# Kernel optimization log

Measured on AMD Instinct MI355X. Metric: run time of the kernel, lower is better.

## Reference

```python
import jax, jax.numpy as jnp
import numpy as np

B, S, H, NH = 4, 2048, 768, 12
HD = H // NH

def _ln(x, g, b, eps=1e-5):
    m = jnp.mean(x, -1, keepdims=True)
    v = jnp.mean((x - m) ** 2, -1, keepdims=True)
    return (x - m) * jax.lax.rsqrt(v + eps) * g + b

def setup_inputs() -> dict:
    key = jax.random.key(0)
    ks = jax.random.split(key, 16)
    s = 0.02
    return {
        "x": jax.random.normal(ks[0], (B, S, H), jnp.float32),
        "prev_state": jax.random.normal(ks[1], (B, S, H), jnp.float32),
        "mask": jax.random.randint(ks[2], (B,), 0, 2).astype(bool),
        # depthwise conv1d (groups=H, k=3): torch weight [H, 1, 3] == OIH
        "conv_dw_w": jax.random.normal(ks[3], (H, 1, 3), jnp.float32) * s,
        "conv_dw_b": jnp.zeros((H,), jnp.float32),
        # pointwise conv1d (k=1) stored as [out, in]
        "conv_pw_w": jax.random.normal(ks[4], (H, H), jnp.float32) * s,
        "conv_pw_b": jnp.zeros((H,), jnp.float32),
        "cn_g": jnp.ones((H,), jnp.float32), "cn_b": jnp.zeros((H,), jnp.float32),
        "Wq": jax.random.normal(ks[5], (H, H), jnp.float32) * s, "bq": jnp.zeros((H,), jnp.float32),
        "Wk": jax.random.normal(ks[6], (H, H), jnp.float32) * s, "bk": jnp.zeros((H,), jnp.float32),
        "Wv": jax.random.normal(ks[7], (H, H), jnp.float32) * s, "bv": jnp.zeros((H,), jnp.float32),
        "Wo": jax.random.normal(ks[8], (H, H), jnp.float32) * s, "bo": jnp.zeros((H,), jnp.float32),
        "pn_g": jnp.ones((H,), jnp.float32), "pn_b": jnp.zeros((H,), jnp.float32),
        "Wpost": jax.random.normal(ks[9], (H, H), jnp.float32) * s, "bpost": jnp.zeros((H,), jnp.float32),
        "Wg": jax.random.normal(ks[10], (1, 2 * H), jnp.float32) * s, "bg": jnp.zeros((1,), jnp.float32),
    }

def reference(x, prev_state, mask, conv_dw_w, conv_dw_b, conv_pw_w, conv_pw_b,
              cn_g, cn_b, Wq, bq, Wk, bk, Wv, bv, Wo, bo,
              pn_g, pn_b, Wpost, bpost, Wg, bg):
    # ---- bridge: depthwise conv (k=3) -> pointwise conv (k=1) -> GELU -> LN ----
    mem_t = prev_state.transpose(0, 2, 1)  # [B, H, S]
    dw = jax.lax.conv_general_dilated(
        mem_t, conv_dw_w, window_strides=(1,), padding=[(1, 1)],
        feature_group_count=H, dimension_numbers=("NCH", "OIH", "NCH")) + conv_dw_b[None, :, None]
    pw = jnp.einsum("bhs,oh->bos", dw, conv_pw_w) + conv_pw_b[None, :, None]
    bridged = jax.nn.gelu(pw, approximate=False).transpose(0, 2, 1)  # [B, S, H]
    bridged = _ln(bridged, cn_g, cn_b)
    # ---- cross attention: q from x, k/v from bridged memory (nope, non-causal) ----
    q = (jnp.einsum("bsh,oh->bso", x, Wq) + bq).reshape(B, S, NH, HD)
    k = (jnp.einsum("bsh,oh->bso", bridged, Wk) + bk).reshape(B, S, NH, HD)
    v = (jnp.einsum("bsh,oh->bso", bridged, Wv) + bv).reshape(B, S, NH, HD)
    scores = jnp.einsum("bqnd,bknd->bnqk", q, k) / np.float32(np.sqrt(HD))
    attn = jax.nn.softmax(scores, axis=-1)
    ao = jnp.einsum("bnqk,bknd->bqnd", attn, v).reshape(B, S, H)
    ao = jnp.einsum("bsh,oh->bso", ao, Wo) + bo
    # ---- post-attn norm, linear, gate, scatter-add back under mask ----
    inj = _ln(ao, pn_g, pn_b)
    inj = jnp.einsum("bsh,oh->bso", inj, Wpost) + bpost
    gate = jax.nn.sigmoid(jnp.einsum("bsh,oh->bso", jnp.concatenate([x, bridged], -1), Wg) + bg)
    gated = gate * jnp.tanh(inj)
    mf = mask.astype(x.dtype)[:, None, None]  # batch-row select == masked scatter-add
    out = x + mf * gated
    # masked MSE aux loss (only over selected rows, as in the original)
    denom = jnp.maximum(mask.sum(), 1).astype(x.dtype) * np.float32(S * H)
    aux = jnp.sum(mf * (bridged - x) ** 2) / denom
    return out, aux
```

## Files before the change

### kernel.cpp

```cpp
#include <hip/hip_runtime.h>
#include <math.h>

#define B_ 4
#define S_ 2048
#define H_ 768
#define NH_ 12
#define HD_ 64
#define BSH (B_ * S_ * H_)
#define NROWS (B_ * S_)
#define WSZ (H_ * H_)

typedef __attribute__((ext_vector_type(8))) short bf16x8;
typedef __attribute__((ext_vector_type(4))) short s16x4;
typedef __attribute__((ext_vector_type(4))) float f32x4;
typedef __attribute__((ext_vector_type(2))) unsigned u32x2;

__device__ __forceinline__ short f2bf(float f) {
  union { float f; unsigned u; } x; x.f = f;
  unsigned r = x.u + 0x7FFF + ((x.u >> 16) & 1);
  return (short)(r >> 16);
}
__device__ __forceinline__ float bf2f(short s) {
  union { unsigned u; float f; } x;
  x.u = ((unsigned)(unsigned short)s) << 16;
  return x.f;
}
__device__ __forceinline__ unsigned bfpack(float lo, float hi) {
  union { float f; unsigned u; } a, b; a.f = lo; b.f = hi;
  return __builtin_amdgcn_perm(b.u, a.u, 0x07060302);
}

typedef __attribute__((address_space(1))) const unsigned int g_u32;
typedef __attribute__((address_space(3))) unsigned int l_u32;
__device__ __forceinline__ void gload16(const void* g, void* l) {
  __builtin_amdgcn_global_load_lds((g_u32*)g, (l_u32*)l, 16, 0, 0);
}

__global__ __launch_bounds__(256) void cvt_x_k(const float* __restrict__ src,
                                               short* __restrict__ dst) {
  int i = (blockIdx.x * 256 + threadIdx.x) * 4;
  float4 v = *(const float4*)(src + i);
  s16x4 o = {f2bf(v.x), f2bf(v.y), f2bf(v.z), f2bf(v.w)};
  *(s16x4*)(dst + i) = o;
}

__global__ __launch_bounds__(256) void cvt6_k(const float* w0, const float* w1,
                                              const float* w2, const float* w3,
                                              const float* w4, const float* w5,
                                              short* __restrict__ dst) {
  int i = (blockIdx.x * 256 + threadIdx.x) * 4;
  int m = i / WSZ;
  int off = i - m * WSZ;
  const float* s = m == 0 ? w0 : m == 1 ? w1 : m == 2 ? w2 : m == 3 ? w3 : m == 4 ? w4 : w5;
  float4 v = *(const float4*)(s + off);
  s16x4 o = {f2bf(v.x), f2bf(v.y), f2bf(v.z), f2bf(v.w)};
  *(s16x4*)(dst + i) = o;
}

__global__ __launch_bounds__(192) void dwconv_k(const float* __restrict__ prev,
                                                const float* __restrict__ w3,
                                                const float* __restrict__ bias,
                                                short* __restrict__ out) {
  int row = blockIdx.x;
  int s = row & (S_ - 1);
  int h = threadIdx.x * 4;
  size_t base = (size_t)row * H_ + h;
  float4 c = *(const float4*)(prev + base);
  float4 wa = *(const float4*)(w3 + h * 3);
  float4 wb = *(const float4*)(w3 + h * 3 + 4);
  float4 wc = *(const float4*)(w3 + h * 3 + 8);
  float4 bi = *(const float4*)(bias + h);
  float4 acc;
  acc.x = bi.x + c.x * wa.y;
  acc.y = bi.y + c.y * wb.x;
  acc.z = bi.z + c.z * wb.w;
  acc.w = bi.w + c.w * wc.z;
  if (s > 0) {
    float4 l = *(const float4*)(prev + base - H_);
    acc.x += l.x * wa.x; acc.y += l.y * wa.w; acc.z += l.z * wb.z; acc.w += l.w * wc.y;
  }
  if (s < S_ - 1) {
    float4 r = *(const float4*)(prev + base + H_);
    acc.x += r.x * wa.z; acc.y += r.y * wb.y; acc.z += r.z * wc.x; acc.w += r.w * wc.w;
  }
  s16x4 o = {f2bf(acc.x), f2bf(acc.y), f2bf(acc.z), f2bf(acc.w)};
  *(s16x4*)(out + base) = o;
}

struct GemmJob {
  const short* A; const short* W; const float* bias; short* C; int act; int tout;
};

__global__ __launch_bounds__(256) void gemm_bf2(GemmJob j0, GemmJob j1, GemmJob j2) {
  GemmJob j = blockIdx.z == 0 ? j0 : (blockIdx.z == 1 ? j1 : j2);
  __shared__ short As[128 * 64];
  __shared__ short Ws[128 * 64];
  int tid = threadIdx.x, lane = tid & 63, w = tid >> 6;
  int wr = w >> 1, wc = w & 1, lm = lane & 15, lq = lane >> 4;
  int m0 = blockIdx.y * 128, n0 = blockIdx.x * 128;
  int srow = lane >> 3;
  int skc = (lane & 7) * 8;
  const short* gA = j.A + (size_t)(m0 + w * 32 + srow) * H_ + skc;
  const short* gW = j.W + (size_t)(n0 + w * 32 + srow) * H_ + skc;
  short* lA = As + w * 2048;
  short* lW = Ws + w * 2048;

  f32x4 acc[4][4];
#pragma unroll
  for (int i = 0; i < 4; ++i)
#pragma unroll
    for (int jj = 0; jj < 4; ++jj) acc[i][jj] = (f32x4){0.f, 0.f, 0.f, 0.f};

  for (int kt = 0; kt < H_; kt += 64) {
    __syncthreads();
#pragma unroll
    for (int c = 0; c < 4; ++c) {
      gload16(gA + kt + (size_t)(c * 8) * H_, lA + c * 512);
      gload16(gW + kt + (size_t)(c * 8) * H_, lW + c * 512);
    }
    __syncthreads();
#pragma unroll
    for (int kk = 0; kk < 2; ++kk) {
      bf16x8 af[4], wf[4];
#pragma unroll
      for (int i = 0; i < 4; ++i)
        af[i] = *(const bf16x8*)&As[(wr * 64 + i * 16 + lm) * 64 + kk * 32 + lq * 8];
#pragma unroll
      for (int jj = 0; jj < 4; ++jj)
        wf[jj] = *(const bf16x8*)&Ws[(wc * 64 + jj * 16 + lm) * 64 + kk * 32 + lq * 8];
#pragma unroll
      for (int i = 0; i < 4; ++i)
#pragma unroll
        for (int jj = 0; jj < 4; ++jj)
          acc[i][jj] = __builtin_amdgcn_mfma_f32_16x16x32_bf16(af[i], wf[jj], acc[i][jj], 0, 0, 0);
    }
  }

  if (!j.tout) {
#pragma unroll
    for (int jj = 0; jj < 4; ++jj) {
      int col = n0 + wc * 64 + jj * 16 + lm;
      float bn = j.bias[col];
#pragma unroll
      for (int i = 0; i < 4; ++i) {
        int mrow = m0 + wr * 64 + i * 16 + lq * 4;
#pragma unroll
        for (int r = 0; r < 4; ++r) {
          float cv = acc[i][jj][r] + bn;
          if (j.act) cv = 0.5f * cv * (1.0f + erff(cv * 0.70710678118f));
          j.C[(size_t)(mrow + r) * H_ + col] = f2bf(cv);
        }
      }
    }
  } else {
    int b = m0 >> 11;
    int sb = (m0 & (S_ - 1)) + wr * 64;
#pragma unroll
    for (int jj = 0; jj < 4; ++jj) {
      int col = n0 + wc * 64 + jj * 16 + lm;
      float bn = j.bias[col];
      short* cp = j.C + ((size_t)(b * H_ + col)) * S_;
#pragma unroll
      for (int i = 0; i < 4; ++i) {
        int s = sb + i * 16 + lq * 4;
        s16x4 pk = {f2bf(acc[i][jj][0] + bn), f2bf(acc[i][jj][1] + bn),
                    f2bf(acc[i][jj][2] + bn), f2bf(acc[i][jj][3] + bn)};
        *(s16x4*)(cp + s) = pk;
      }
    }
  }
}

__global__ __launch_bounds__(256) void ln_bf(const short* __restrict__ X,
                                             short* __restrict__ Y,
                                             const float* __restrict__ g,
                                             const float* __restrict__ bb) {
  int row = blockIdx.x;
  size_t base = (size_t)row * H_;
  int h0 = threadIdx.x, h1 = h0 + 256, h2 = h0 + 512;
  float x0 = bf2f(X[base + h0]), x1 = bf2f(X[base + h1]), x2 = bf2f(X[base + h2]);
  float s = x0 + x1 + x2;
  float s2 = x0 * x0 + x1 * x1 + x2 * x2;
  for (int off = 32; off > 0; off >>= 1) {
    s += __shfl_down(s, off);
    s2 += __shfl_down(s2, off);
  }
  __shared__ float sa[4], sq[4], st[2];
  int wid = threadIdx.x >> 6, lane = threadIdx.x & 63;
  if (lane == 0) { sa[wid] = s; sq[wid] = s2; }
  __syncthreads();
  if (threadIdx.x == 0) {
    float ts = sa[0] + sa[1] + sa[2] + sa[3];
    float ts2 = sq[0] + sq[1] + sq[2] + sq[3];
    float mean = ts * (1.0f / H_);
    float var = ts2 * (1.0f / H_) - mean * mean;
    st[0] = mean;
    st[1] = rsqrtf(var + 1e-5f);
  }
  __syncthreads();
  float mean = st[0], rstd = st[1];
  Y[base + h0] = f2bf((x0 - mean) * rstd * g[h0] + bb[h0]);
  Y[base + h1] = f2bf((x1 - mean) * rstd * g[h1] + bb[h1]);
  Y[base + h2] = f2bf((x2 - mean) * rstd * g[h2] + bb[h2]);
}

__global__ __launch_bounds__(512) void attn3_k(const short* __restrict__ qb,
                                               const short* __restrict__ kb,
                                               const short* __restrict__ vtb,
                                               short* __restrict__ aob) {
  __shared__ short Ks[64 * 72];
  __shared__ short Vt[64 * 72];
  __shared__ short Ps[8 * 16 * 72];
  int tid = threadIdx.x, lane = tid & 63, w = tid >> 6;
  int lm = lane & 15, lq = lane >> 4;
  int b = blockIdx.z, n = blockIdx.y, q0 = blockIdx.x * 128;
  int hoff = n * HD_;

  const short* qrow = qb + ((size_t)(b * S_ + q0 + w * 16 + lm)) * H_ + hoff;
  bf16x8 qf0 = *(const bf16x8*)(qrow + lq * 8);
  bf16x8 qf1 = *(const bf16x8*)(qrow + 32 + lq * 8);

  float l_ = 0.f;
  f32x4 o[4];
#pragma unroll
  for (int i = 0; i < 4; ++i) o[i] = (f32x4){0.f, 0.f, 0.f, 0.f};

  int r0 = tid >> 3, c0 = (tid & 7) * 8;
  const short* kg = kb + ((size_t)(b * S_)) * H_ + hoff;
  const short* vg = vtb + ((size_t)(b * H_ + hoff)) * S_;
  const float C1 = 0.1803368802f;

  bf16x8 kv = *(const bf16x8*)(kg + (size_t)r0 * H_ + c0);
  bf16x8 vv = *(const bf16x8*)(vg + (size_t)r0 * S_ + c0);

  for (int kt = 0; kt < S_; kt += 64) {
    __syncthreads();
    *(bf16x8*)&Ks[r0 * 72 + c0] = kv;
    *(bf16x8*)&Vt[r0 * 72 + c0] = vv;
    __syncthreads();
    if (kt + 64 < S_) {
      kv = *(const bf16x8*)(kg + (size_t)(kt + 64 + r0) * H_ + c0);
      vv = *(const bf16x8*)(vg + (size_t)r0 * S_ + kt + 64 + c0);
    }

    f32x4 st[4];
#pragma unroll
    for (int ni = 0; ni < 4; ++ni) {
      bf16x8 ka0 = *(const bf16x8*)&Ks[(ni * 16 + lm) * 72 + lq * 8];
      bf16x8 ka1 = *(const bf16x8*)&Ks[(ni * 16 + lm) * 72 + 32 + lq * 8];
      f32x4 z = (f32x4){0.f, 0.f, 0.f, 0.f};
      z = __builtin_amdgcn_mfma_f32_16x16x32_bf16(ka0, qf0, z, 0, 0, 0);
      st[ni] = __builtin_amdgcn_mfma_f32_16x16x32_bf16(ka1, qf1, z, 0, 0, 0);
    }

    float rs = 0.f;
#pragma unroll
    for (int ni = 0; ni < 4; ++ni) {
      float p0 = exp2f(st[ni][0] * C1);
      float p1 = exp2f(st[ni][1] * C1);
      float p2 = exp2f(st[ni][2] * C1);
      float p3 = exp2f(st[ni][3] * C1);
      rs += (p0 + p1) + (p2 + p3);
      u32x2 pk = {bfpack(p0, p1), bfpack(p2, p3)};
      *(u32x2*)&Ps[(w * 16 + lm) * 72 + ni * 16 + lq * 4] = pk;
    }
    rs += __shfl_xor(rs, 16);
    rs += __shfl_xor(rs, 32);
    l_ += rs;

    bf16x8 pf0 = *(const bf16x8*)&Ps[(w * 16 + lm) * 72 + lq * 8];
    bf16x8 pf1 = *(const bf16x8*)&Ps[(w * 16 + lm) * 72 + 32 + lq * 8];
#pragma unroll
    for (int nd = 0; nd < 4; ++nd) {
      bf16x8 va0 = *(const bf16x8*)&Vt[(nd * 16 + lm) * 72 + lq * 8];
      bf16x8 va1 = *(const bf16x8*)&Vt[(nd * 16 + lm) * 72 + 32 + lq * 8];
      o[nd] = __builtin_amdgcn_mfma_f32_16x16x32_bf16(va0, pf0, o[nd], 0, 0, 0);
      o[nd] = __builtin_amdgcn_mfma_f32_16x16x32_bf16(va1, pf1, o[nd], 0, 0, 0);
    }
  }

  float inv = 1.0f / l_;
  short* orow = aob + ((size_t)(b * S_ + q0 + w * 16 + lm)) * H_ + hoff;
#pragma unroll
  for (int nd = 0; nd < 4; ++nd) {
    s16x4 pk = {f2bf(o[nd][0] * inv), f2bf(o[nd][1] * inv),
                f2bf(o[nd][2] * inv), f2bf(o[nd][3] * inv)};
    *(s16x4*)(orow + nd * 16 + lq * 4) = pk;
  }
}

__global__ __launch_bounds__(192) void gate_out_k(const float* __restrict__ x,
                                                  const short* __restrict__ br,
                                                  const short* __restrict__ inj,
                                                  const int* __restrict__ mask,
                                                  const float* __restrict__ Wg,
                                                  const float* __restrict__ bg,
                                                  float* __restrict__ out,
                                                  float* __restrict__ paux) {
  int row = blockIdx.x;
  int b = row >> 11;
  size_t base = (size_t)row * H_;
  int h = threadIdx.x * 4;
  float4 xv = *(const float4*)(x + base + h);
  s16x4 brv = *(const s16x4*)(br + base + h);
  s16x4 inv = *(const s16x4*)(inj + base + h);
  float4 wg0 = *(const float4*)(Wg + h);
  float4 wg1 = *(const float4*)(Wg + H_ + h);
  float b0 = bf2f(brv.x), b1 = bf2f(brv.y), b2 = bf2f(brv.z), b3 = bf2f(brv.w);
  float dot = xv.x * wg0.x + xv.y * wg0.y + xv.z * wg0.z + xv.w * wg0.w
            + b0 * wg1.x + b1 * wg1.y + b2 * wg1.z + b3 * wg1.w;
  float d0 = b0 - xv.x, d1 = b1 - xv.y, d2 = b2 - xv.z, d3 = b3 - xv.w;
  float aux = d0 * d0 + d1 * d1 + d2 * d2 + d3 * d3;
  for (int off = 32; off > 0; off >>= 1) {
    dot += __shfl_down(dot, off);
    aux += __shfl_down(aux, off);
  }
  __shared__ float sd[3], sx[3], gsh[2];
  int wid = threadIdx.x >> 6, lane = threadIdx.x & 63;
  if (lane == 0) { sd[wid] = dot; sx[wid] = aux; }
  __syncthreads();
  if (threadIdx.x == 0) {
    float td = sd[0] + sd[1] + sd[2];
    float ta = sx[0] + sx[1] + sx[2];
    gsh[0] = 1.0f / (1.0f + expf(-(td + bg[0])));
    gsh[1] = ta;
  }
  __syncthreads();
  float mf = (mask[b] != 0) ? 1.0f : 0.0f;
  float gm = gsh[0] * mf;
  float v0 = bf2f(inv.x), v1 = bf2f(inv.y), v2 = bf2f(inv.z), v3 = bf2f(inv.w);
  float e0 = __expf(2.f * v0), e1 = __expf(2.f * v1), e2 = __expf(2.f * v2), e3 = __expf(2.f * v3);
  float4 ov;
  ov.x = xv.x + gm * ((e0 - 1.f) / (e0 + 1.f));
  ov.y = xv.y + gm * ((e1 - 1.f) / (e1 + 1.f));
  ov.z = xv.z + gm * ((e2 - 1.f) / (e2 + 1.f));
  ov.w = xv.w + gm * ((e3 - 1.f) / (e3 + 1.f));
  *(float4*)(out + base + h) = ov;
  if (threadIdx.x == 0) paux[row] = mf * gsh[1];
}

__global__ __launch_bounds__(256) void aux_reduce_k(const float* __restrict__ paux,
                                                    const int* __restrict__ mask,
                                                    float* __restrict__ outp) {
  float s = 0.f;
  for (int i = threadIdx.x; i < NROWS; i += 256) s += paux[i];
  for (int off = 32; off > 0; off >>= 1) s += __shfl_down(s, off);
  __shared__ float sw[4];
  int wid = threadIdx.x >> 6, lane = threadIdx.x & 63;
  if (lane == 0) sw[wid] = s;
  __syncthreads();
  if (threadIdx.x == 0) {
    float t = sw[0] + sw[1] + sw[2] + sw[3];
    int nm = (mask[0] != 0) + (mask[1] != 0) + (mask[2] != 0) + (mask[3] != 0);
    if (nm < 1) nm = 1;
    outp[0] = t / ((float)nm * (float)(S_ * H_));
  }
}

extern "C" void kernel_launch(void* const* d_in, const int* in_sizes, int n_in,
                              void* d_out, int out_size, void* d_ws, size_t ws_size,
                              hipStream_t stream) {
  const float* x     = (const float*)d_in[0];
  const float* prev  = (const float*)d_in[1];
  const int*   mask  = (const int*)d_in[2];
  const float* dw_w  = (const float*)d_in[3];
  const float* dw_b  = (const float*)d_in[4];
  const float* pw_w  = (const float*)d_in[5];
  const float* pw_b  = (const float*)d_in[6];
  const float* cn_g  = (const float*)d_in[7];
  const float* cn_b  = (const float*)d_in[8];
  const float* Wq    = (const float*)d_in[9];
  const float* bq    = (const float*)d_in[10];
  const float* Wk    = (const float*)d_in[11];
  const float* bk    = (const float*)d_in[12];
  const float* Wv    = (const float*)d_in[13];
  const float* bv    = (const float*)d_in[14];
  const float* Wo    = (const float*)d_in[15];
  const float* bo    = (const float*)d_in[16];
  const float* pn_g  = (const float*)d_in[17];
  const float* pn_b  = (const float*)d_in[18];
  const float* Wpost = (const float*)d_in[19];
  const float* bpost = (const float*)d_in[20];
  const float* Wg    = (const float*)d_in[21];
  const float* bg    = (const float*)d_in[22];
  float* out = (float*)d_out;

  short* B0 = (short*)d_ws;
  short* B1 = B0 + BSH;
  short* B2 = B1 + BSH;
  short* B3 = B2 + BSH;
  short* B4 = B3 + BSH;
  short* B5 = B4 + BSH;
  short* WW = B5 + BSH;
  float* paux = (float*)(WW + 6 * WSZ);

  dim3 g1(H_ / 128, NROWS / 128, 1);
  dim3 g3(H_ / 128, NROWS / 128, 3);

  GemmJob jpw   = {B1, WW,           pw_b,  B2, 1, 0};
  GemmJob jq    = {B0, WW + WSZ,     bq,    B1, 0, 0};
  GemmJob jk    = {B3, WW + 2 * WSZ, bk,    B4, 0, 0};
  GemmJob jv    = {B3, WW + 3 * WSZ, bv,    B5, 0, 1};
  GemmJob jo    = {B2, WW + 4 * WSZ, bo,    B4, 0, 0};
  GemmJob jpost = {B4, WW + 5 * WSZ, bpost, B5, 0, 0};

  cvt6_k<<<6 * WSZ / 1024, 256, 0, stream>>>(pw_w, Wq, Wk, Wv, Wo, Wpost, WW);
  cvt_x_k<<<BSH / 1024, 256, 0, stream>>>(x, B0);
  dwconv_k<<<NROWS, 192, 0, stream>>>(prev, dw_w, dw_b, B1);
  gemm_bf2<<<g1, 256, 0, stream>>>(jpw, jpw, jpw);
  ln_bf<<<NROWS, 256, 0, stream>>>(B2, B3, cn_g, cn_b);
  gemm_bf2<<<g3, 256, 0, stream>>>(jq, jk, jv);
  attn3_k<<<dim3(S_ / 128, NH_, B_), 512, 0, stream>>>(B1, B4, B5, B2);
  gemm_bf2<<<g1, 256, 0, stream>>>(jo, jo, jo);
  ln_bf<<<NROWS, 256, 0, stream>>>(B4, B4, pn_g, pn_b);
  gemm_bf2<<<g1, 256, 0, stream>>>(jpost, jpost, jpost);
  gate_out_k<<<NROWS, 192, 0, stream>>>(x, B3, B5, mask, Wg, bg, out, paux);
  aux_reduce_k<<<1, 256, 0, stream>>>(paux, mask, out + BSH);
}
```

Before: 419.2 us.

## Add 128x64 GEMM tile for single GEMMs and double query rows per attention wave

```diff
diff --git a/kernel.cpp b/kernel.cpp
--- a/kernel.cpp
+++ b/kernel.cpp
@@ -171,6 +171,69 @@
   }
 }
 
+__global__ __launch_bounds__(256) void gemm_n64(const short* __restrict__ A,
+                                                const short* __restrict__ W,
+                                                const float* __restrict__ bias,
+                                                short* __restrict__ C, int act) {
+  __shared__ short As[128 * 64];
+  __shared__ short Ws[64 * 64];
+  int tid = threadIdx.x, lane = tid & 63, w = tid >> 6;
+  int wm = w >> 1, wn = w & 1, lm = lane & 15, lq = lane >> 4;
+  int m0 = blockIdx.y * 128, n0 = blockIdx.x * 64;
+  const short* gA = A + (size_t)(m0 + w * 32 + (lane >> 3)) * H_ + (lane & 7) * 8;
+  const short* gW = W + (size_t)(n0 + w * 16 + (lane >> 3)) * H_ + (lane & 7) * 8;
+  short* lA = As + w * 2048;
+  short* lW = Ws + w * 1024;
+
+  f32x4 acc[4][2];
+#pragma unroll
+  for (int i = 0; i < 4; ++i)
+#pragma unroll
+    for (int jj = 0; jj < 2; ++jj) acc[i][jj] = (f32x4){0.f, 0.f, 0.f, 0.f};
+
+  for (int kt = 0; kt < H_; kt += 64) {
+    __syncthreads();
+#pragma unroll
+    for (int c = 0; c < 4; ++c)
+      gload16(gA + kt + (size_t)(c * 8) * H_, lA + c * 512);
+#pragma unroll
+    for (int c = 0; c < 2; ++c)
+      gload16(gW + kt + (size_t)(c * 8) * H_, lW + c * 512);
+    __syncthreads();
+#pragma unroll
+    for (int kk = 0; kk < 2; ++kk) {
+      bf16x8 af[4], wf[2];
+#pragma unroll
+      for (int i = 0; i < 4; ++i)
+        af[i] = *(const bf16x8*)&As[(wm * 64 + i * 16 + lm) * 64 + kk * 32 + lq * 8];
+#pragma unroll
+      for (int jj = 0; jj < 2; ++jj)
+        wf[jj] = *(const bf16x8*)&Ws[(wn * 32 + jj * 16 + lm) * 64 + kk * 32 + lq * 8];
+#pragma unroll
+      for (int i = 0; i < 4; ++i)
+#pragma unroll
+        for (int jj = 0; jj < 2; ++jj)
+          acc[i][jj] = __builtin_amdgcn_mfma_f32_16x16x32_bf16(af[i], wf[jj], acc[i][jj], 0, 0, 0);
+    }
+  }
+
+#pragma unroll
+  for (int jj = 0; jj < 2; ++jj) {
+    int col = n0 + wn * 32 + jj * 16 + lm;
+    float bn = bias[col];
+#pragma unroll
+    for (int i = 0; i < 4; ++i) {
+      int mrow = m0 + wm * 64 + i * 16 + lq * 4;
+#pragma unroll
+      for (int r = 0; r < 4; ++r) {
+        float cv = acc[i][jj][r] + bn;
+        if (act) cv = 0.5f * cv * (1.0f + erff(cv * 0.70710678118f));
+        C[(size_t)(mrow + r) * H_ + col] = f2bf(cv);
+      }
+    }
+  }
+}
+
 __global__ __launch_bounds__(256) void ln_bf(const short* __restrict__ X,
                                              short* __restrict__ Y,
                                              const float* __restrict__ g,
@@ -204,88 +267,116 @@
   Y[base + h2] = f2bf((x2 - mean) * rstd * g[h2] + bb[h2]);
 }
 
-__global__ __launch_bounds__(512) void attn3_k(const short* __restrict__ qb,
+__global__ __launch_bounds__(256) void attn4_k(const short* __restrict__ qb,
                                                const short* __restrict__ kb,
                                                const short* __restrict__ vtb,
                                                short* __restrict__ aob) {
   __shared__ short Ks[64 * 72];
   __shared__ short Vt[64 * 72];
-  __shared__ short Ps[8 * 16 * 72];
+  __shared__ short Ps[128 * 72];
   int tid = threadIdx.x, lane = tid & 63, w = tid >> 6;
   int lm = lane & 15, lq = lane >> 4;
   int b = blockIdx.z, n = blockIdx.y, q0 = blockIdx.x * 128;
   int hoff = n * HD_;
 
-  const short* qrow = qb + ((size_t)(b * S_ + q0 + w * 16 + lm)) * H_ + hoff;
-  bf16x8 qf0 = *(const bf16x8*)(qrow + lq * 8);
-  bf16x8 qf1 = *(const bf16x8*)(qrow + 32 + lq * 8);
-
-  float l_ = 0.f;
-  f32x4 o[4];
-#pragma unroll
-  for (int i = 0; i < 4; ++i) o[i] = (f32x4){0.f, 0.f, 0.f, 0.f};
-
-  int r0 = tid >> 3, c0 = (tid & 7) * 8;
+  bf16x8 qf[2][2];
+#pragma unroll
+  for (int qg = 0; qg < 2; ++qg) {
+    const short* qrow = qb + ((size_t)(b * S_ + q0 + w * 32 + qg * 16 + lm)) * H_ + hoff;
+    qf[qg][0] = *(const bf16x8*)(qrow + lq * 8);
+    qf[qg][1] = *(const bf16x8*)(qrow + 32 + lq * 8);
+  }
+
+  float l_[2] = {0.f, 0.f};
+  f32x4 o[4][2];
+#pragma unroll
+  for (int i = 0; i < 4; ++i)
+#pragma unroll
+    for (int qg = 0; qg < 2; ++qg) o[i][qg] = (f32x4){0.f, 0.f, 0.f, 0.f};
+
+  int r0 = tid >> 2, c0 = (tid & 3) * 16;
   const short* kg = kb + ((size_t)(b * S_)) * H_ + hoff;
   const short* vg = vtb + ((size_t)(b * H_ + hoff)) * S_;
   const float C1 = 0.1803368802f;
 
-  bf16x8 kv = *(const bf16x8*)(kg + (size_t)r0 * H_ + c0);
-  bf16x8 vv = *(const bf16x8*)(vg + (size_t)r0 * S_ + c0);
+  bf16x8 kv0 = *(const bf16x8*)(kg + (size_t)r0 * H_ + c0);
+  bf16x8 kv1 = *(const bf16x8*)(kg + (size_t)r0 * H_ + c0 + 8);
+  bf16x8 vv0 = *(const bf16x8*)(vg + (size_t)r0 * S_ + c0);
+  bf16x8 vv1 = *(const bf16x8*)(vg + (size_t)r0 * S_ + c0 + 8);
 
   for (int kt = 0; kt < S_; kt += 64) {
     __syncthreads();
-    *(bf16x8*)&Ks[r0 * 72 + c0] = kv;
-    *(bf16x8*)&Vt[r0 * 72 + c0] = vv;
+    *(bf16x8*)&Ks[r0 * 72 + c0] = kv0;
+    *(bf16x8*)&Ks[r0 * 72 + c0 + 8] = kv1;
+    *(bf16x8*)&Vt[r0 * 72 + c0] = vv0;
+    *(bf16x8*)&Vt[r0 * 72 + c0 + 8] = vv1;
     __syncthreads();
     if (kt + 64 < S_) {
-      kv = *(const bf16x8*)(kg + (size_t)(kt + 64 + r0) * H_ + c0);
-      vv = *(const bf16x8*)(vg + (size_t)r0 * S_ + kt + 64 + c0);
-    }
-
-    f32x4 st[4];
+      kv0 = *(const bf16x8*)(kg + (size_t)(kt + 64 + r0) * H_ + c0);
+      kv1 = *(const bf16x8*)(kg + (size_t)(kt + 64 + r0) * H_ + c0 + 8);
+      vv0 = *(const bf16x8*)(vg + (size_t)r0 * S_ + kt + 64 + c0);
+      vv1 = *(const bf16x8*)(vg + (size_t)r0 * S_ + kt + 64 + c0 + 8);
+    }
+
+    f32x4 st[4][2];
 #pragma unroll
     for (int ni = 0; ni < 4; ++ni) {
       bf16x8 ka0 = *(const bf16x8*)&Ks[(ni * 16 + lm) * 72 + lq * 8];
       bf16x8 ka1 = *(const bf16x8*)&Ks[(ni * 16 + lm) * 72 + 32 + lq * 8];
-      f32x4 z = (f32x4){0.f, 0.f, 0.f, 0.f};
-      z = __builtin_amdgcn_mfma_f32_16x16x32_bf16(ka0, qf0, z, 0, 0, 0);
-      st[ni] = __builtin_amdgcn_mfma_f32_16x16x32_bf16(ka1, qf1, z, 0, 0, 0);
-    }
-
-    float rs = 0.f;
-#pragma unroll
-    for (int ni = 0; ni < 4; ++ni) {
-      float p0 = exp2f(st[ni][0] * C1);
-      float p1 = exp2f(st[ni][1] * C1);
-      float p2 = exp2f(st[ni][2] * C1);
-      float p3 = exp2f(st[ni][3] * C1);
-      rs += (p0 + p1) + (p2 + p3);
-      u32x2 pk = {bfpack(p0, p1), bfpack(p2, p3)};
-      *(u32x2*)&Ps[(w * 16 + lm) * 72 + ni * 16 + lq * 4] = pk;
-    }
-    rs += __shfl_xor(rs, 16);
-    rs += __shfl_xor(rs, 32);
-    l_ += rs;
-
-    bf16x8 pf0 = *(const bf16x8*)&Ps[(w * 16 + lm) * 72 + lq * 8];
-    bf16x8 pf1 = *(const bf16x8*)&Ps[(w * 16 + lm) * 72 + 32 + lq * 8];
+#pragma unroll
+      for (int qg = 0; qg < 2; ++qg) {
+        f32x4 z = (f32x4){0.f, 0.f, 0.f, 0.f};
+        z = __builtin_amdgcn_mfma_f32_16x16x32_bf16(ka0, qf[qg][0], z, 0, 0, 0);
+        st[ni][qg] = __builtin_amdgcn_mfma_f32_16x16x32_bf16(ka1, qf[qg][1], z, 0, 0, 0);
+      }
+    }
+
+#pragma unroll
+    for (int qg = 0; qg < 2; ++qg) {
+      float rs = 0.f;
+#pragma unroll
+      for (int ni = 0; ni < 4; ++ni) {
+        float p0 = exp2f(st[ni][qg][0] * C1);
+        float p1 = exp2f(st[ni][qg][1] * C1);
+        float p2 = exp2f(st[ni][qg][2] * C1);
+        float p3 = exp2f(st[ni][qg][3] * C1);
+        rs += (p0 + p1) + (p2 + p3);
+        u32x2 pk = {bfpack(p0, p1), bfpack(p2, p3)};
+        *(u32x2*)&Ps[(w * 32 + qg * 16 + lm) * 72 + ni * 16 + lq * 4] = pk;
+      }
+      rs += __shfl_xor(rs, 16);
+      rs += __shfl_xor(rs, 32);
+      l_[qg] += rs;
+    }
+
+    bf16x8 pf[2][2];
+#pragma unroll
+    for (int qg = 0; qg < 2; ++qg) {
+      pf[qg][0] = *(const bf16x8*)&Ps[(w * 32 + qg * 16 + lm) * 72 + lq * 8];
+      pf[qg][1] = *(const bf16x8*)&Ps[(w * 32 + qg * 16 + lm) * 72 + 32 + lq * 8];
+    }
 #pragma unroll
     for (int nd = 0; nd < 4; ++nd) {
       bf16x8 va0 = *(const bf16x8*)&Vt[(nd * 16 + lm) * 72 + lq * 8];
       bf16x8 va1 = *(const bf16x8*)&Vt[(nd * 16 + lm) * 72 + 32 + lq * 8];
-      o[nd] = __builtin_amdgcn_mfma_f32_16x16x32_bf16(va0, pf0, o[nd], 0, 0, 0);
-      o[nd] = __builtin_amdgcn_mfma_f32_16x16x32_bf16(va1, pf1, o[nd], 0, 0, 0);
-    }
-  }
-
-  float inv = 1.0f / l_;
-  short* orow = aob + ((size_t)(b * S_ + q0 + w * 16 + lm)) * H_ + hoff;
-#pragma unroll
-  for (int nd = 0; nd < 4; ++nd) {
-    s16x4 pk = {f2bf(o[nd][0] * inv), f2bf(o[nd][1] * inv),
-                f2bf(o[nd][2] * inv), f2bf(o[nd][3] * inv)};
-    *(s16x4*)(orow + nd * 16 + lq * 4) = pk;
+#pragma unroll
+      for (int qg = 0; qg < 2; ++qg) {
+        o[nd][qg] = __builtin_amdgcn_mfma_f32_16x16x32_bf16(va0, pf[qg][0], o[nd][qg], 0, 0, 0);
+        o[nd][qg] = __builtin_amdgcn_mfma_f32_16x16x32_bf16(va1, pf[qg][1], o[nd][qg], 0, 0, 0);
+      }
+    }
+  }
+
+#pragma unroll
+  for (int qg = 0; qg < 2; ++qg) {
+    float inv = 1.0f / l_[qg];
+    short* orow = aob + ((size_t)(b * S_ + q0 + w * 32 + qg * 16 + lm)) * H_ + hoff;
+#pragma unroll
+    for (int nd = 0; nd < 4; ++nd) {
+      s16x4 pk = {f2bf(o[nd][qg][0] * inv), f2bf(o[nd][qg][1] * inv),
+                  f2bf(o[nd][qg][2] * inv), f2bf(o[nd][qg][3] * inv)};
+      *(s16x4*)(orow + nd * 16 + lq * 4) = pk;
+    }
   }
 }
 
@@ -394,26 +485,23 @@
   short* WW = B5 + BSH;
   float* paux = (float*)(WW + 6 * WSZ);
 
-  dim3 g1(H_ / 128, NROWS / 128, 1);
   dim3 g3(H_ / 128, NROWS / 128, 3);
-
-  GemmJob jpw   = {B1, WW,           pw_b,  B2, 1, 0};
-  GemmJob jq    = {B0, WW + WSZ,     bq,    B1, 0, 0};
-  GemmJob jk    = {B3, WW + 2 * WSZ, bk,    B4, 0, 0};
-  GemmJob jv    = {B3, WW + 3 * WSZ, bv,    B5, 0, 1};
-  GemmJob jo    = {B2, WW + 4 * WSZ, bo,    B4, 0, 0};
-  GemmJob jpost = {B4, WW + 5 * WSZ, bpost, B5, 0, 0};
+  dim3 gn(H_ / 64, NROWS / 128, 1);
+
+  GemmJob jq = {B0, WW + WSZ,     bq, B1, 0, 0};
+  GemmJob jk = {B3, WW + 2 * WSZ, bk, B4, 0, 0};
+  GemmJob jv = {B3, WW + 3 * WSZ, bv, B5, 0, 1};
 
   cvt6_k<<<6 * WSZ / 1024, 256, 0, stream>>>(pw_w, Wq, Wk, Wv, Wo, Wpost, WW);
   cvt_x_k<<<BSH / 1024, 256, 0, stream>>>(x, B0);
   dwconv_k<<<NROWS, 192, 0, stream>>>(prev, dw_w, dw_b, B1);
-  gemm_bf2<<<g1, 256, 0, stream>>>(jpw, jpw, jpw);
+  gemm_n64<<<gn, 256, 0, stream>>>(B1, WW, pw_b, B2, 1);
   ln_bf<<<NROWS, 256, 0, stream>>>(B2, B3, cn_g, cn_b);
   gemm_bf2<<<g3, 256, 0, stream>>>(jq, jk, jv);
-  attn3_k<<<dim3(S_ / 128, NH_, B_), 512, 0, stream>>>(B1, B4, B5, B2);
-  gemm_bf2<<<g1, 256, 0, stream>>>(jo, jo, jo);
+  attn4_k<<<dim3(S_ / 128, NH_, B_), 256, 0, stream>>>(B1, B4, B5, B2);
+  gemm_n64<<<gn, 256, 0, stream>>>(B2, WW + 4 * WSZ, bo, B4, 0);
   ln_bf<<<NROWS, 256, 0, stream>>>(B4, B4, pn_g, pn_b);
-  gemm_bf2<<<g1, 256, 0, stream>>>(jpost, jpost, jpost);
+  gemm_n64<<<gn, 256, 0, stream>>>(B4, WW + 5 * WSZ, bpost, B5, 0);
   gate_out_k<<<NROWS, 192, 0, stream>>>(x, B3, B5, mask, Wg, bg, out, paux);
   aux_reduce_k<<<1, 256, 0, stream>>>(paux, mask, out + BSH);
 }
```

After: 413.5 us. About the same (-1.4%).
